# Performance work log

Hardware: AMD Instinct MI355X
Metric: run time of the kernel (lower is better)

The kernel has to match this reference:

```python
import jax, jax.numpy as jnp
import numpy as np

TOP_K = 2


def setup_inputs() -> dict:
    key = jax.random.key(0)
    ks = jax.random.split(key, 5)
    T, D, F, E = 1024, 1024, 2048, 16
    scale_d = 1.0 / np.sqrt(D)
    scale_f = 1.0 / np.sqrt(F)
    return {
        "x_TD": jax.random.normal(ks[0], (T, D), jnp.float32),
        "router_w_DE": jax.random.normal(ks[1], (D, E), jnp.float32) * scale_d,
        "kernel_gating_EDF": jax.random.normal(ks[2], (E, D, F), jnp.float32) * scale_d,
        "kernel_up_EDF": jax.random.normal(ks[3], (E, D, F), jnp.float32) * scale_d,
        "kernel_down_EFD": jax.random.normal(ks[4], (E, F, D), jnp.float32) * scale_f,
    }


def _router(x_TD, router_w_DE):
    # linear router -> softmax -> top-k, renormalized weights
    logits_TE = x_TD @ router_w_DE
    probs_TE = jax.nn.softmax(logits_TE, axis=-1)
    weights_TX, indices_TX = jax.lax.top_k(probs_TE, TOP_K)
    weights_TX = weights_TX / jnp.sum(weights_TX, axis=-1, keepdims=True)
    return weights_TX, indices_TX


def reference(x_TD, router_w_DE, kernel_gating_EDF, kernel_up_EDF, kernel_down_EFD):
    E = kernel_gating_EDF.shape[0]
    weights_TX, indices_TX = _router(x_TD, router_w_DE)
    # scatter top-k weights into a dense (T, E) combine matrix via one-hot
    one_hot_TXE = jax.nn.one_hot(indices_TX, E, dtype=x_TD.dtype)
    full_weights_TE = jnp.sum(one_hot_TXE * weights_TX[..., None], axis=1)
    # dense all-experts MoE (as in _moe_fwd)
    gating_TEF = jnp.einsum("TD,EDF->TEF", x_TD, kernel_gating_EDF)
    up_TEF = jnp.einsum("TD,EDF->TEF", x_TD, kernel_up_EDF)
    fuse_TEF = jax.nn.silu(gating_TEF) * up_TEF
    down_TED = jnp.einsum("TEF,EFD->TED", fuse_TEF, kernel_down_EFD)
    out_TD = jnp.einsum("TED,TE->TD", down_TED, full_weights_TE)
    return out_TD.astype(x_TD.dtype)
```

## Files before the change

kernel.cpp:

```cpp
#include <hip/hip_runtime.h>
#include <hip/hip_bf16.h>

typedef __bf16 bf16_t;
typedef __bf16 bf16x8 __attribute__((ext_vector_type(8)));
typedef __bf16 bf16x4 __attribute__((ext_vector_type(4)));
typedef float  f32x4  __attribute__((ext_vector_type(4)));

#define T_TOK 1024
#define DDIM  1024
#define FDIM  2048
#define NEXP  16
#define MAXR  192

#define WS_ENTRY_OFF   1024
#define WS_ENTRYW_OFF  66560
#define WS_XG_OFF      132096
#define WS_PART_OFF    132096
#define WS_FUSE_OFF    8520704

#define GLL16(g, l) __builtin_amdgcn_global_load_lds(                      \
    (const __attribute__((address_space(1))) unsigned int*)(g),            \
    (__attribute__((address_space(3))) unsigned int*)(l), 16, 0, 0)

__global__ __launch_bounds__(64) void router_kernel(
    const float* __restrict__ x, const float* __restrict__ rw,
    int* __restrict__ cnt, int* __restrict__ entry, float* __restrict__ entry_w)
{
    const int t = blockIdx.x;
    const int lane = threadIdx.x;
    float acc[NEXP];
#pragma unroll
    for (int e = 0; e < NEXP; ++e) acc[e] = 0.f;
#pragma unroll
    for (int i = 0; i < DDIM / 64; ++i) {
        const int d = lane + i * 64;
        const float xv = x[(size_t)t * DDIM + d];
        const float* r = rw + (size_t)d * NEXP;
#pragma unroll
        for (int e = 0; e < NEXP; ++e) acc[e] += xv * r[e];
    }
#pragma unroll
    for (int e = 0; e < NEXP; ++e) {
        float v = acc[e];
        for (int off = 32; off > 0; off >>= 1) v += __shfl_down(v, off);
        acc[e] = v;
    }
    if (lane == 0) {
        int i0 = -1, i1 = -1;
        float v0 = -1e30f, v1 = -1e30f;
#pragma unroll
        for (int e = 0; e < NEXP; ++e) {
            const float v = acc[e];
            if (v > v0)      { v1 = v0; i1 = i0; v0 = v; i0 = e; }
            else if (v > v1) { v1 = v;  i1 = e; }
        }
        const float e1 = __expf(v1 - v0);
        const float w0 = 1.f / (1.f + e1);
        const float w1 = e1 / (1.f + e1);
        int p = atomicAdd(&cnt[i0], 1);
        entry[i0 * T_TOK + p] = t * 2 + 0;
        entry_w[i0 * T_TOK + p] = w0;
        p = atomicAdd(&cnt[i1], 1);
        entry[i1 * T_TOK + p] = t * 2 + 1;
        entry_w[i1 * T_TOK + p] = w1;
    }
}

__global__ __launch_bounds__(256) void gather_kernel(
    const float* __restrict__ x, const int* __restrict__ cnt,
    const int* __restrict__ entry, bf16_t* __restrict__ xg)
{
    const int e  = blockIdx.x;
    const int i0 = blockIdx.y * 32;
    const int tid = threadIdx.x;
    int n_tok = cnt[e]; if (n_tok > MAXR) n_tok = MAXR;
    for (int rr = 0; rr < 32; ++rr) {
        const int i = i0 + rr;
        bf16x4 v4;
        v4[0] = (bf16_t)0.f; v4[1] = (bf16_t)0.f; v4[2] = (bf16_t)0.f; v4[3] = (bf16_t)0.f;
        if (i < n_tok) {
            const int tok = entry[e * T_TOK + i] >> 1;
            const float4 v = *(const float4*)(x + (size_t)tok * DDIM + tid * 4);
            v4[0] = (bf16_t)v.x; v4[1] = (bf16_t)v.y; v4[2] = (bf16_t)v.z; v4[3] = (bf16_t)v.w;
        }
        *(bf16x4*)(xg + ((size_t)e * MAXR + i) * DDIM + tid * 4) = v4;
    }
}

__global__ __launch_bounds__(256, 2) void ffn1_kernel(
    const bf16_t* __restrict__ xg,
    const float* __restrict__ wg, const float* __restrict__ wu,
    const int* __restrict__ cnt, const int* __restrict__ entry,
    bf16_t* __restrict__ fuse)
{
    const int e  = blockIdx.x;
    const int f0 = blockIdx.y * 64;
    int n_tok = cnt[e]; if (n_tok > MAXR) n_tok = MAXR;

    __shared__ __align__(16) bf16_t As[2][MAXR][32];
    __shared__ __align__(16) bf16_t Bgs[2][64][40];
    __shared__ __align__(16) bf16_t Bus[2][64][40];
    __shared__ int sem[MAXR];

    const int tid  = threadIdx.x;
    const int wave = tid >> 6;
    const int lane = tid & 63;
    const int r    = lane & 15;
    const int q    = lane >> 4;

    const bf16_t* xg_e = xg + (size_t)e * MAXR * DDIM;
    const float* wg_p = wg + (size_t)e * DDIM * FDIM + (size_t)(wave * 8) * FDIM + f0 + lane;
    const float* wu_p = wu + (size_t)e * DDIM * FDIM + (size_t)(wave * 8) * FDIM + f0 + lane;

    if (tid < MAXR) sem[tid] = (tid < n_tok) ? entry[e * T_TOK + tid] : -1;

    float rg[8], ru[8];
#pragma unroll
    for (int j = 0; j < 8; ++j) { rg[j] = wg_p[(size_t)j * FDIM]; ru[j] = wu_p[(size_t)j * FDIM]; }
#pragma unroll
    for (int c = 0; c < 3; ++c) {
        const int rowb = wave * 48 + c * 16;
        const bf16_t* g = xg_e + (size_t)(rowb + (lane >> 2)) * DDIM + (lane & 3) * 8;
        GLL16(g, &As[0][rowb][0] + lane * 8);
    }

    f32x4 accg[3][4], accu[3][4];
#pragma unroll
    for (int a = 0; a < 3; ++a)
#pragma unroll
        for (int b = 0; b < 4; ++b) {
            accg[a][b] = (f32x4){0.f, 0.f, 0.f, 0.f};
            accu[a][b] = (f32x4){0.f, 0.f, 0.f, 0.f};
        }

    for (int i = 0; i < 32; ++i) {
        const int buf = i & 1;
        bf16x8 pg, pu;
#pragma unroll
        for (int j = 0; j < 8; ++j) { pg[j] = (bf16_t)rg[j]; pu[j] = (bf16_t)ru[j]; }
        *(bf16x8*)&Bgs[buf][lane][wave * 8] = pg;
        *(bf16x8*)&Bus[buf][lane][wave * 8] = pu;
        __syncthreads();
        if (i < 31) {
            wg_p += (size_t)32 * FDIM; wu_p += (size_t)32 * FDIM;
#pragma unroll
            for (int j = 0; j < 8; ++j) { rg[j] = wg_p[(size_t)j * FDIM]; ru[j] = wu_p[(size_t)j * FDIM]; }
            const int kk = (i + 1) * 32;
#pragma unroll
            for (int c = 0; c < 3; ++c) {
                const int rowb = wave * 48 + c * 16;
                const bf16_t* g = xg_e + (size_t)(rowb + (lane >> 2)) * DDIM + kk + (lane & 3) * 8;
                GLL16(g, &As[buf ^ 1][rowb][0] + lane * 8);
            }
        }
        bf16x8 af[3];
#pragma unroll
        for (int mt = 0; mt < 3; ++mt)
            af[mt] = *(const bf16x8*)&As[buf][wave * 48 + mt * 16 + r][q * 8];
        bf16x8 bg[4], bu[4];
#pragma unroll
        for (int nt = 0; nt < 4; ++nt) {
            bg[nt] = *(const bf16x8*)&Bgs[buf][nt * 16 + r][q * 8];
            bu[nt] = *(const bf16x8*)&Bus[buf][nt * 16 + r][q * 8];
        }
#pragma unroll
        for (int mt = 0; mt < 3; ++mt)
#pragma unroll
            for (int nt = 0; nt < 4; ++nt) {
                accg[mt][nt] = __builtin_amdgcn_mfma_f32_16x16x32_bf16(af[mt], bg[nt], accg[mt][nt], 0, 0, 0);
                accu[mt][nt] = __builtin_amdgcn_mfma_f32_16x16x32_bf16(af[mt], bu[nt], accu[mt][nt], 0, 0, 0);
            }
    }

    bf16_t* fuse_e = fuse + (size_t)e * MAXR * FDIM + f0;
#pragma unroll
    for (int mt = 0; mt < 3; ++mt) {
#pragma unroll
        for (int j = 0; j < 4; ++j) {
            const int m = wave * 48 + mt * 16 + q * 4 + j;
            const bool valid = sem[m] >= 0;
            bf16_t* dst = fuse_e + (size_t)m * FDIM;
#pragma unroll
            for (int nt = 0; nt < 4; ++nt) {
                const float g = accg[mt][nt][j];
                const float u = accu[mt][nt][j];
                const float h = valid ? (g / (1.f + __expf(-g))) * u : 0.f;
                dst[nt * 16 + r] = (bf16_t)h;
            }
        }
    }
}

__global__ __launch_bounds__(256, 2) void ffn2_kernel(
    const bf16_t* __restrict__ fuse, const float* __restrict__ wd,
    const int* __restrict__ cnt, const int* __restrict__ entry,
    const float* __restrict__ entry_w, float* __restrict__ partial)
{
    const int e  = blockIdx.x;
    const int d0 = blockIdx.y * 32;
    int n_tok = cnt[e]; if (n_tok > MAXR) n_tok = MAXR;

    __shared__ __align__(16) bf16_t As[2][2][MAXR][32];
    __shared__ __align__(16) bf16_t Bs[2][32][72];
    __shared__ int   sem[MAXR];
    __shared__ float sw[MAXR];

    const int tid  = threadIdx.x;
    const int wave = tid >> 6;
    const int lane = tid & 63;
    const int r    = lane & 15;
    const int q    = lane >> 4;

    const bf16_t* fu_e = fuse + (size_t)e * MAXR * FDIM;
    const int bn = tid & 31;
    const int k8 = (tid >> 5) * 8;
    const float* wd_p = wd + (size_t)e * FDIM * DDIM + (size_t)k8 * DDIM + d0 + bn;

    if (tid < MAXR) {
        sem[tid] = (tid < n_tok) ? entry[e * T_TOK + tid] : -1;
        sw[tid]  = (tid < n_tok) ? entry_w[e * T_TOK + tid] : 0.f;
    }

    float rb[8];
#pragma unroll
    for (int j = 0; j < 8; ++j) rb[j] = wd_p[(size_t)j * DDIM];
#pragma unroll
    for (int ks = 0; ks < 2; ++ks)
#pragma unroll
        for (int c = 0; c < 3; ++c) {
            const int rowb = wave * 48 + c * 16;
            const bf16_t* g = fu_e + (size_t)(rowb + (lane >> 2)) * FDIM + ks * 32 + (lane & 3) * 8;
            GLL16(g, &As[0][ks][rowb][0] + lane * 8);
        }

    f32x4 acc[3][2];
#pragma unroll
    for (int a = 0; a < 3; ++a)
#pragma unroll
        for (int b = 0; b < 2; ++b) acc[a][b] = (f32x4){0.f, 0.f, 0.f, 0.f};

    for (int i = 0; i < 32; ++i) {
        const int buf = i & 1;
        bf16x8 pb;
#pragma unroll
        for (int j = 0; j < 8; ++j) pb[j] = (bf16_t)rb[j];
        *(bf16x8*)&Bs[buf][bn][k8] = pb;
        __syncthreads();
        if (i < 31) {
            wd_p += (size_t)64 * DDIM;
#pragma unroll
            for (int j = 0; j < 8; ++j) rb[j] = wd_p[(size_t)j * DDIM];
            const int kk = (i + 1) * 64;
#pragma unroll
            for (int ks = 0; ks < 2; ++ks)
#pragma unroll
                for (int c = 0; c < 3; ++c) {
                    const int rowb = wave * 48 + c * 16;
                    const bf16_t* g = fu_e + (size_t)(rowb + (lane >> 2)) * FDIM + kk + ks * 32 + (lane & 3) * 8;
                    GLL16(g, &As[buf ^ 1][ks][rowb][0] + lane * 8);
                }
        }
#pragma unroll
        for (int ks = 0; ks < 2; ++ks) {
            bf16x8 af[3], bb[2];
#pragma unroll
            for (int mt = 0; mt < 3; ++mt)
                af[mt] = *(const bf16x8*)&As[buf][ks][wave * 48 + mt * 16 + r][q * 8];
#pragma unroll
            for (int nt = 0; nt < 2; ++nt)
                bb[nt] = *(const bf16x8*)&Bs[buf][nt * 16 + r][ks * 32 + q * 8];
#pragma unroll
            for (int mt = 0; mt < 3; ++mt)
#pragma unroll
                for (int nt = 0; nt < 2; ++nt)
                    acc[mt][nt] = __builtin_amdgcn_mfma_f32_16x16x32_bf16(af[mt], bb[nt], acc[mt][nt], 0, 0, 0);
        }
    }

#pragma unroll
    for (int mt = 0; mt < 3; ++mt) {
#pragma unroll
        for (int j = 0; j < 4; ++j) {
            const int m = wave * 48 + mt * 16 + q * 4 + j;
            const int em = sem[m];
            if (em < 0) continue;
            const int t = em >> 1;
            const int slot = em & 1;
            const float w = sw[m];
            float* dst = partial + ((size_t)slot * T_TOK + t) * DDIM + d0;
#pragma unroll
            for (int nt = 0; nt < 2; ++nt)
                dst[nt * 16 + r] = acc[mt][nt][j] * w;
        }
    }
}

__global__ __launch_bounds__(256) void add_kernel(
    const float* __restrict__ partial, float* __restrict__ out)
{
    const int i = blockIdx.x * blockDim.x + threadIdx.x;
    const float4 a = ((const float4*)partial)[i];
    const float4 b = ((const float4*)(partial + (size_t)T_TOK * DDIM))[i];
    float4 o;
    o.x = a.x + b.x; o.y = a.y + b.y; o.z = a.z + b.z; o.w = a.w + b.w;
    ((float4*)out)[i] = o;
}

extern "C" void kernel_launch(void* const* d_in, const int* in_sizes, int n_in,
                              void* d_out, int out_size, void* d_ws, size_t ws_size,
                              hipStream_t stream) {
    const float* x  = (const float*)d_in[0];
    const float* rw = (const float*)d_in[1];
    const float* wg = (const float*)d_in[2];
    const float* wu = (const float*)d_in[3];
    const float* wd = (const float*)d_in[4];
    float* out = (float*)d_out;

    char* ws = (char*)d_ws;
    int*    cnt     = (int*)ws;
    int*    entry   = (int*)(ws + WS_ENTRY_OFF);
    float*  entry_w = (float*)(ws + WS_ENTRYW_OFF);
    bf16_t* xg      = (bf16_t*)(ws + WS_XG_OFF);
    float*  partial = (float*)(ws + WS_PART_OFF);
    bf16_t* fuse    = (bf16_t*)(ws + WS_FUSE_OFF);

    hipMemsetAsync(cnt, 0, 64, stream);

    router_kernel<<<T_TOK, 64, 0, stream>>>(x, rw, cnt, entry, entry_w);

    gather_kernel<<<dim3(NEXP, MAXR / 32), 256, 0, stream>>>(x, cnt, entry, xg);

    ffn1_kernel<<<dim3(NEXP, FDIM / 64), 256, 0, stream>>>(
        xg, wg, wu, cnt, entry, fuse);

    ffn2_kernel<<<dim3(NEXP, DDIM / 32), 256, 0, stream>>>(
        fuse, wd, cnt, entry, entry_w, partial);

    add_kernel<<<(T_TOK * DDIM / 4) / 256, 256, 0, stream>>>(partial, out);
}
```

Baseline: 443.8 us.

## Shrink FFN tiles, split-K the down projection, load activations directly into registers

ffn1 now processes 32 F columns per block instead of 64, so its grid doubles. Each block stages gate and up weights through one shared buffer split between two thread halves. The x-gather rows are read straight from global memory into registers, replacing the LDS async copy, and the valid-row masking is dropped. ffn2 splits the F reduction into two halves over a third grid dimension and combines them with atomicAdd into a partial buffer that is zeroed by a new memset. Occupancy hints go up to 4 blocks per SIMD and the gather grid is made finer. The aim is more parallelism across the weight-streaming kernels; the cost is atomics, an extra memset, and padded rows now producing nonzero fuse values, though ffn2 ignores those rows.

```diff
diff --git a/kernel.cpp b/kernel.cpp
--- a/kernel.cpp
+++ b/kernel.cpp
@@ -17,10 +17,6 @@
 #define WS_XG_OFF      132096
 #define WS_PART_OFF    132096
 #define WS_FUSE_OFF    8520704
-
-#define GLL16(g, l) __builtin_amdgcn_global_load_lds(                      \
-    (const __attribute__((address_space(1))) unsigned int*)(g),            \
-    (__attribute__((address_space(3))) unsigned int*)(l), 16, 0, 0)
 
 __global__ __launch_bounds__(64) void router_kernel(
     const float* __restrict__ x, const float* __restrict__ rw,
@@ -71,10 +67,11 @@
     const int* __restrict__ entry, bf16_t* __restrict__ xg)
 {
     const int e  = blockIdx.x;
-    const int i0 = blockIdx.y * 32;
+    const int i0 = blockIdx.y * 8;
     const int tid = threadIdx.x;
     int n_tok = cnt[e]; if (n_tok > MAXR) n_tok = MAXR;
-    for (int rr = 0; rr < 32; ++rr) {
+#pragma unroll
+    for (int rr = 0; rr < 8; ++rr) {
         const int i = i0 + rr;
         bf16x4 v4;
         v4[0] = (bf16_t)0.f; v4[1] = (bf16_t)0.f; v4[2] = (bf16_t)0.f; v4[3] = (bf16_t)0.f;
@@ -87,20 +84,15 @@
     }
 }
 
-__global__ __launch_bounds__(256, 2) void ffn1_kernel(
+__global__ __launch_bounds__(256, 4) void ffn1_kernel(
     const bf16_t* __restrict__ xg,
     const float* __restrict__ wg, const float* __restrict__ wu,
-    const int* __restrict__ cnt, const int* __restrict__ entry,
     bf16_t* __restrict__ fuse)
 {
     const int e  = blockIdx.x;
-    const int f0 = blockIdx.y * 64;
-    int n_tok = cnt[e]; if (n_tok > MAXR) n_tok = MAXR;
-
-    __shared__ __align__(16) bf16_t As[2][MAXR][32];
-    __shared__ __align__(16) bf16_t Bgs[2][64][40];
-    __shared__ __align__(16) bf16_t Bus[2][64][40];
-    __shared__ int sem[MAXR];
+    const int f0 = blockIdx.y * 32;
+
+    __shared__ __align__(16) bf16_t Bs[2][2][32][40];
 
     const int tid  = threadIdx.x;
     const int wave = tid >> 6;
@@ -108,99 +100,89 @@
     const int r    = lane & 15;
     const int q    = lane >> 4;
 
-    const bf16_t* xg_e = xg + (size_t)e * MAXR * DDIM;
-    const float* wg_p = wg + (size_t)e * DDIM * FDIM + (size_t)(wave * 8) * FDIM + f0 + lane;
-    const float* wu_p = wu + (size_t)e * DDIM * FDIM + (size_t)(wave * 8) * FDIM + f0 + lane;
-
-    if (tid < MAXR) sem[tid] = (tid < n_tok) ? entry[e * T_TOK + tid] : -1;
-
-    float rg[8], ru[8];
-#pragma unroll
-    for (int j = 0; j < 8; ++j) { rg[j] = wg_p[(size_t)j * FDIM]; ru[j] = wu_p[(size_t)j * FDIM]; }
-#pragma unroll
-    for (int c = 0; c < 3; ++c) {
-        const int rowb = wave * 48 + c * 16;
-        const bf16_t* g = xg_e + (size_t)(rowb + (lane >> 2)) * DDIM + (lane & 3) * 8;
-        GLL16(g, &As[0][rowb][0] + lane * 8);
-    }
-
-    f32x4 accg[3][4], accu[3][4];
+    const int mat  = tid >> 7;
+    const int bn   = tid & 31;
+    const int koct = (tid >> 5) & 3;
+    const float* w_p = (mat ? wu : wg) + (size_t)e * DDIM * FDIM
+                     + (size_t)(koct * 8) * FDIM + f0 + bn;
+
+    const bf16_t* xg_e = xg + (size_t)e * MAXR * DDIM + q * 8;
+
+    float rb[8];
+#pragma unroll
+    for (int j = 0; j < 8; ++j) rb[j] = w_p[(size_t)j * FDIM];
+
+    bf16x8 af[2][3];
+#pragma unroll
+    for (int mt = 0; mt < 3; ++mt)
+        af[0][mt] = *(const bf16x8*)(xg_e + (size_t)(wave * 48 + mt * 16 + r) * DDIM);
+
+    f32x4 accg[3][2], accu[3][2];
 #pragma unroll
     for (int a = 0; a < 3; ++a)
 #pragma unroll
-        for (int b = 0; b < 4; ++b) {
+        for (int b = 0; b < 2; ++b) {
             accg[a][b] = (f32x4){0.f, 0.f, 0.f, 0.f};
             accu[a][b] = (f32x4){0.f, 0.f, 0.f, 0.f};
         }
 
     for (int i = 0; i < 32; ++i) {
         const int buf = i & 1;
-        bf16x8 pg, pu;
-#pragma unroll
-        for (int j = 0; j < 8; ++j) { pg[j] = (bf16_t)rg[j]; pu[j] = (bf16_t)ru[j]; }
-        *(bf16x8*)&Bgs[buf][lane][wave * 8] = pg;
-        *(bf16x8*)&Bus[buf][lane][wave * 8] = pu;
+        bf16x8 pb;
+#pragma unroll
+        for (int j = 0; j < 8; ++j) pb[j] = (bf16_t)rb[j];
+        *(bf16x8*)&Bs[buf][mat][bn][koct * 8] = pb;
         __syncthreads();
         if (i < 31) {
-            wg_p += (size_t)32 * FDIM; wu_p += (size_t)32 * FDIM;
-#pragma unroll
-            for (int j = 0; j < 8; ++j) { rg[j] = wg_p[(size_t)j * FDIM]; ru[j] = wu_p[(size_t)j * FDIM]; }
+            w_p += (size_t)32 * FDIM;
+#pragma unroll
+            for (int j = 0; j < 8; ++j) rb[j] = w_p[(size_t)j * FDIM];
             const int kk = (i + 1) * 32;
 #pragma unroll
-            for (int c = 0; c < 3; ++c) {
-                const int rowb = wave * 48 + c * 16;
-                const bf16_t* g = xg_e + (size_t)(rowb + (lane >> 2)) * DDIM + kk + (lane & 3) * 8;
-                GLL16(g, &As[buf ^ 1][rowb][0] + lane * 8);
+            for (int mt = 0; mt < 3; ++mt)
+                af[buf ^ 1][mt] = *(const bf16x8*)(xg_e + (size_t)(wave * 48 + mt * 16 + r) * DDIM + kk);
+        }
+        bf16x8 bg[2], bu[2];
+#pragma unroll
+        for (int nt = 0; nt < 2; ++nt) {
+            bg[nt] = *(const bf16x8*)&Bs[buf][0][nt * 16 + r][q * 8];
+            bu[nt] = *(const bf16x8*)&Bs[buf][1][nt * 16 + r][q * 8];
+        }
+#pragma unroll
+        for (int mt = 0; mt < 3; ++mt)
+#pragma unroll
+            for (int nt = 0; nt < 2; ++nt) {
+                accg[mt][nt] = __builtin_amdgcn_mfma_f32_16x16x32_bf16(af[buf][mt], bg[nt], accg[mt][nt], 0, 0, 0);
+                accu[mt][nt] = __builtin_amdgcn_mfma_f32_16x16x32_bf16(af[buf][mt], bu[nt], accu[mt][nt], 0, 0, 0);
             }
-        }
-        bf16x8 af[3];
-#pragma unroll
-        for (int mt = 0; mt < 3; ++mt)
-            af[mt] = *(const bf16x8*)&As[buf][wave * 48 + mt * 16 + r][q * 8];
-        bf16x8 bg[4], bu[4];
-#pragma unroll
-        for (int nt = 0; nt < 4; ++nt) {
-            bg[nt] = *(const bf16x8*)&Bgs[buf][nt * 16 + r][q * 8];
-            bu[nt] = *(const bf16x8*)&Bus[buf][nt * 16 + r][q * 8];
-        }
-#pragma unroll
-        for (int mt = 0; mt < 3; ++mt)
-#pragma unroll
-            for (int nt = 0; nt < 4; ++nt) {
-                accg[mt][nt] = __builtin_amdgcn_mfma_f32_16x16x32_bf16(af[mt], bg[nt], accg[mt][nt], 0, 0, 0);
-                accu[mt][nt] = __builtin_amdgcn_mfma_f32_16x16x32_bf16(af[mt], bu[nt], accu[mt][nt], 0, 0, 0);
-            }
     }
 
     bf16_t* fuse_e = fuse + (size_t)e * MAXR * FDIM + f0;
 #pragma unroll
-    for (int mt = 0; mt < 3; ++mt) {
+    for (int mt = 0; mt < 3; ++mt)
 #pragma unroll
         for (int j = 0; j < 4; ++j) {
             const int m = wave * 48 + mt * 16 + q * 4 + j;
-            const bool valid = sem[m] >= 0;
-            bf16_t* dst = fuse_e + (size_t)m * FDIM;
-#pragma unroll
-            for (int nt = 0; nt < 4; ++nt) {
+#pragma unroll
+            for (int nt = 0; nt < 2; ++nt) {
                 const float g = accg[mt][nt][j];
                 const float u = accu[mt][nt][j];
-                const float h = valid ? (g / (1.f + __expf(-g))) * u : 0.f;
-                dst[nt * 16 + r] = (bf16_t)h;
+                const float h = (g / (1.f + __expf(-g))) * u;
+                fuse_e[(size_t)m * FDIM + nt * 16 + r] = (bf16_t)h;
             }
         }
-    }
-}
-
-__global__ __launch_bounds__(256, 2) void ffn2_kernel(
+}
+
+__global__ __launch_bounds__(256, 4) void ffn2_kernel(
     const bf16_t* __restrict__ fuse, const float* __restrict__ wd,
     const int* __restrict__ cnt, const int* __restrict__ entry,
     const float* __restrict__ entry_w, float* __restrict__ partial)
 {
     const int e  = blockIdx.x;
     const int d0 = blockIdx.y * 32;
+    const int kh = blockIdx.z;
     int n_tok = cnt[e]; if (n_tok > MAXR) n_tok = MAXR;
 
-    __shared__ __align__(16) bf16_t As[2][2][MAXR][32];
     __shared__ __align__(16) bf16_t Bs[2][32][72];
     __shared__ int   sem[MAXR];
     __shared__ float sw[MAXR];
@@ -211,10 +193,11 @@
     const int r    = lane & 15;
     const int q    = lane >> 4;
 
-    const bf16_t* fu_e = fuse + (size_t)e * MAXR * FDIM;
-    const int bn = tid & 31;
-    const int k8 = (tid >> 5) * 8;
-    const float* wd_p = wd + (size_t)e * FDIM * DDIM + (size_t)k8 * DDIM + d0 + bn;
+    const int bn   = tid & 31;
+    const int koct = tid >> 5;
+    const float* wd_p = wd + (size_t)e * FDIM * DDIM
+                      + (size_t)(kh * 1024 + koct * 8) * DDIM + d0 + bn;
+    const bf16_t* fu_e = fuse + (size_t)e * MAXR * FDIM + kh * 1024 + q * 8;
 
     if (tid < MAXR) {
         sem[tid] = (tid < n_tok) ? entry[e * T_TOK + tid] : -1;
@@ -224,14 +207,13 @@
     float rb[8];
 #pragma unroll
     for (int j = 0; j < 8; ++j) rb[j] = wd_p[(size_t)j * DDIM];
-#pragma unroll
-    for (int ks = 0; ks < 2; ++ks)
-#pragma unroll
-        for (int c = 0; c < 3; ++c) {
-            const int rowb = wave * 48 + c * 16;
-            const bf16_t* g = fu_e + (size_t)(rowb + (lane >> 2)) * FDIM + ks * 32 + (lane & 3) * 8;
-            GLL16(g, &As[0][ks][rowb][0] + lane * 8);
-        }
+
+    bf16x8 af[2][2][3];
+#pragma unroll
+    for (int s = 0; s < 2; ++s)
+#pragma unroll
+        for (int mt = 0; mt < 3; ++mt)
+            af[0][s][mt] = *(const bf16x8*)(fu_e + (size_t)(wave * 48 + mt * 16 + r) * FDIM + s * 32);
 
     f32x4 acc[3][2];
 #pragma unroll
@@ -239,46 +221,40 @@
 #pragma unroll
         for (int b = 0; b < 2; ++b) acc[a][b] = (f32x4){0.f, 0.f, 0.f, 0.f};
 
-    for (int i = 0; i < 32; ++i) {
+    for (int i = 0; i < 16; ++i) {
         const int buf = i & 1;
         bf16x8 pb;
 #pragma unroll
         for (int j = 0; j < 8; ++j) pb[j] = (bf16_t)rb[j];
-        *(bf16x8*)&Bs[buf][bn][k8] = pb;
+        *(bf16x8*)&Bs[buf][bn][koct * 8] = pb;
         __syncthreads();
-        if (i < 31) {
+        if (i < 15) {
             wd_p += (size_t)64 * DDIM;
 #pragma unroll
             for (int j = 0; j < 8; ++j) rb[j] = wd_p[(size_t)j * DDIM];
             const int kk = (i + 1) * 64;
 #pragma unroll
-            for (int ks = 0; ks < 2; ++ks)
-#pragma unroll
-                for (int c = 0; c < 3; ++c) {
-                    const int rowb = wave * 48 + c * 16;
-                    const bf16_t* g = fu_e + (size_t)(rowb + (lane >> 2)) * FDIM + kk + ks * 32 + (lane & 3) * 8;
-                    GLL16(g, &As[buf ^ 1][ks][rowb][0] + lane * 8);
-                }
-        }
-#pragma unroll
-        for (int ks = 0; ks < 2; ++ks) {
-            bf16x8 af[3], bb[2];
+            for (int s = 0; s < 2; ++s)
+#pragma unroll
+                for (int mt = 0; mt < 3; ++mt)
+                    af[buf ^ 1][s][mt] = *(const bf16x8*)(fu_e + (size_t)(wave * 48 + mt * 16 + r) * FDIM + kk + s * 32);
+        }
+#pragma unroll
+        for (int s = 0; s < 2; ++s) {
+            bf16x8 bb[2];
+#pragma unroll
+            for (int nt = 0; nt < 2; ++nt)
+                bb[nt] = *(const bf16x8*)&Bs[buf][nt * 16 + r][s * 32 + q * 8];
 #pragma unroll
             for (int mt = 0; mt < 3; ++mt)
-                af[mt] = *(const bf16x8*)&As[buf][ks][wave * 48 + mt * 16 + r][q * 8];
-#pragma unroll
-            for (int nt = 0; nt < 2; ++nt)
-                bb[nt] = *(const bf16x8*)&Bs[buf][nt * 16 + r][ks * 32 + q * 8];
-#pragma unroll
-            for (int mt = 0; mt < 3; ++mt)
 #pragma unroll
                 for (int nt = 0; nt < 2; ++nt)
-                    acc[mt][nt] = __builtin_amdgcn_mfma_f32_16x16x32_bf16(af[mt], bb[nt], acc[mt][nt], 0, 0, 0);
-        }
-    }
-
-#pragma unroll
-    for (int mt = 0; mt < 3; ++mt) {
+                    acc[mt][nt] = __builtin_amdgcn_mfma_f32_16x16x32_bf16(af[buf][s][mt], bb[nt], acc[mt][nt], 0, 0, 0);
+        }
+    }
+
+#pragma unroll
+    for (int mt = 0; mt < 3; ++mt)
 #pragma unroll
         for (int j = 0; j < 4; ++j) {
             const int m = wave * 48 + mt * 16 + q * 4 + j;
@@ -290,9 +266,8 @@
             float* dst = partial + ((size_t)slot * T_TOK + t) * DDIM + d0;
 #pragma unroll
             for (int nt = 0; nt < 2; ++nt)
-                dst[nt * 16 + r] = acc[mt][nt][j] * w;
-        }
-    }
+                atomicAdd(&dst[nt * 16 + r], acc[mt][nt][j] * w);
+        }
 }
 
 __global__ __launch_bounds__(256) void add_kernel(
@@ -328,12 +303,13 @@
 
     router_kernel<<<T_TOK, 64, 0, stream>>>(x, rw, cnt, entry, entry_w);
 
-    gather_kernel<<<dim3(NEXP, MAXR / 32), 256, 0, stream>>>(x, cnt, entry, xg);
-
-    ffn1_kernel<<<dim3(NEXP, FDIM / 64), 256, 0, stream>>>(
-        xg, wg, wu, cnt, entry, fuse);
-
-    ffn2_kernel<<<dim3(NEXP, DDIM / 32), 256, 0, stream>>>(
+    gather_kernel<<<dim3(NEXP, MAXR / 8), 256, 0, stream>>>(x, cnt, entry, xg);
+
+    ffn1_kernel<<<dim3(NEXP, FDIM / 32), 256, 0, stream>>>(xg, wg, wu, fuse);
+
+    hipMemsetAsync(partial, 0, (size_t)2 * T_TOK * DDIM * sizeof(float), stream);
+
+    ffn2_kernel<<<dim3(NEXP, DDIM / 32, 2), 256, 0, stream>>>(
         fuse, wd, cnt, entry, entry_w, partial);
 
     add_kernel<<<(T_TOK * DDIM / 4) / 256, 256, 0, stream>>>(partial, out);
```

New measurement: 479.3 us. +8.0%, slower.
